# Optimization experiments

Hardware: AMD Instinct MI355X
Metric: run time of the kernel (lower is better)

Reference implementation:

```python
import jax, jax.numpy as jnp
import numpy as np
import math

EMBED_DIM = 1024
NUM_HEADS = 16
HEAD_DIM = EMBED_DIM // NUM_HEADS
BLOCK_SIZE = 64
NUM_RAND_BLOCKS = 3
B, L = 2, 2048


def _build_sparse_mask(seq_len, block_size, num_rand_blocks, seed=0):
    """BigBird block-sparse mask: global (first/last block) + window (prev/self/next) + random blocks."""
    nb = seq_len // block_size
    bm = np.zeros((nb, nb), dtype=bool)
    # global: first and last blocks attend to all / are attended by all
    bm[0, :] = True
    bm[:, 0] = True
    bm[-1, :] = True
    bm[:, -1] = True
    # sliding window for interior blocks
    for b in range(1, nb - 1):
        bm[b, max(b - 1, 0):b + 2] = True
    # random blocks for interior blocks (deterministic for reproducibility)
    rng = np.random.default_rng(seed)
    for b in range(1, nb - 1):
        avail = [x for x in range(nb) if x != b]
        picks = rng.permutation(len(avail))[:num_rand_blocks]
        for p in picks:
            bm[b, avail[p]] = True
    # expand block mask to token-level [L, L]
    return np.kron(bm, np.ones((block_size, block_size), dtype=bool))


def setup_inputs() -> dict:
    key = jax.random.key(0)
    k0, k1, k2, k3, k4 = jax.random.split(key, 5)
    hidden_states = jax.random.normal(k0, (B, L, EMBED_DIM), dtype=jnp.float32)
    s = 0.02
    # torch nn.Linear weights have shape [out_features, in_features]
    Wq = jax.random.normal(k1, (EMBED_DIM, EMBED_DIM), dtype=jnp.float32) * s
    Wk = jax.random.normal(k2, (EMBED_DIM, EMBED_DIM), dtype=jnp.float32) * s
    Wv = jax.random.normal(k3, (EMBED_DIM, EMBED_DIM), dtype=jnp.float32) * s
    Wo = jax.random.normal(k4, (EMBED_DIM, EMBED_DIM), dtype=jnp.float32) * s
    sparse_mask = jnp.asarray(_build_sparse_mask(L, BLOCK_SIZE, NUM_RAND_BLOCKS))
    return {"hidden_states": hidden_states, "Wq": Wq, "Wk": Wk, "Wv": Wv,
            "Wo": Wo, "sparse_mask": sparse_mask}


def reference(hidden_states, Wq, Wk, Wv, Wo, sparse_mask):
    Bsz, Lq, D = hidden_states.shape
    H, hd = NUM_HEADS, HEAD_DIM
    # projections (Linear no bias): x @ W.T
    q = (hidden_states @ Wq.T).reshape(Bsz, Lq, H, hd).transpose(0, 2, 1, 3)
    k = (hidden_states @ Wk.T).reshape(Bsz, Lq, H, hd).transpose(0, 2, 1, 3)
    v = (hidden_states @ Wv.T).reshape(Bsz, Lq, H, hd).transpose(0, 2, 1, 3)
    # dense scores with block-sparse mask (matches reference module's math)
    scores = jnp.einsum('bhqd,bhkd->bhqk', q, k) / math.sqrt(hd)  # [B,H,L,L]
    scores = jnp.where(sparse_mask[None, None, :, :], scores, -jnp.inf)
    attn = jax.nn.softmax(scores.astype(jnp.float32), axis=-1).astype(scores.dtype)
    out = jnp.einsum('bhqk,bhkd->bhqd', attn, v)
    out = out.transpose(0, 2, 1, 3).reshape(Bsz, Lq, D)
    out = out @ Wo.T
    return out
```

## Files before the change

kernel.cpp:

```cpp
#include <hip/hip_runtime.h>
#include <hip/hip_bf16.h>
#include <stdint.h>

#define LSEQ   2048
#define DMODEL 1024
#define NHEADS 16
#define HDIM   64
#define NB     32
#define BATCH  2
#define NGRP   38
#define NWG_ATTN (32 * NGRP)

typedef unsigned short u16;
typedef __attribute__((ext_vector_type(8))) __bf16 bf16x8;
typedef __attribute__((ext_vector_type(4))) float f32x4;
typedef __attribute__((ext_vector_type(4))) unsigned int u32x4;
typedef __attribute__((ext_vector_type(4))) u16 u16x4;


__device__ __forceinline__ u16 f2b(float f) {
  unsigned b = __float_as_uint(f);
  return (u16)((b + 0x7FFFu + ((b >> 16) & 1u)) >> 16);
}

__device__ __forceinline__ void lds_dma16(const u16* g, u16* l) {
  __builtin_amdgcn_global_load_lds(
      (__attribute__((address_space(1))) const void*)g,
      (__attribute__((address_space(3))) void*)l, 16, 0, 0);
}

__device__ __forceinline__ bool probe_is_bf16(const void* src) {
  const u16* p = (const u16*)src;
  int cnt = 0;
  #pragma unroll
  for (int i = 0; i < 64; ++i) {
    int e = (p[i] >> 7) & 0xFF;
    cnt += (e >= 100 && e <= 140) ? 1 : 0;
  }
  return cnt >= 48;
}

__device__ __forceinline__ bool mask_block(const void* m, int qb, int kb) {
  const unsigned char* p = (const unsigned char*)m;
  size_t e = (size_t)(qb * 64) * LSEQ + (size_t)kb * 64;
  unsigned char b0 = p[0], b1 = p[1], b2 = p[2];
  if (b0 == 1 && b1 == 1) return p[e] != 0;
  if (b0 == 1 && b1 == 0 && b2 == 1) return ((const u16*)m)[e] != 0;
  if (b0 == 1) return ((const unsigned int*)m)[e] != 0;
  if (b0 == 0x80 && b1 == 0x3f) return ((const u16*)m)[e] != 0;
  return ((const float*)m)[e] != 0.0f;
}

__global__ __launch_bounds__(256) void convert_kernel(
    const void* __restrict__ hs, const void* __restrict__ wq,
    const void* __restrict__ wk, const void* __restrict__ wv,
    const void* __restrict__ wo, u16* __restrict__ dst,
    const void* __restrict__ mask, int* __restrict__ skb,
    f32x4* __restrict__ zbuf, int zn4) {
  __shared__ int sflag;
  if (threadIdx.x == 0) sflag = probe_is_bf16(hs) ? 1 : 0;
  __syncthreads();
  bool isbf = sflag != 0;
  if (blockIdx.x == 0 && threadIdx.x < NB) {
    int qb = threadIdx.x;
    int base = (qb == 0) ? 0 : ((qb == 31) ? 32 : (64 + (qb - 1) * 8));
    int cap = (qb == 0 || qb == 31) ? 32 : 8;
    int c = 0;
    for (int kb = 0; kb < NB; ++kb)
      if (mask_block(mask, qb, kb)) skb[base + c++] = kb;
    for (; c < cap; ++c) skb[base + c] = -1;
  }
  const int HS4 = BATCH * LSEQ * DMODEL / 4;
  const int W4 = DMODEL * DMODEL / 4;
  int total4 = HS4 + 4 * W4;
  int stride = gridDim.x * blockDim.x;
  for (int i = blockIdx.x * blockDim.x + threadIdx.x; i < total4; i += stride) {
    const void* src;
    int off;
    if (i < HS4) { src = hs; off = i; }
    else {
      int j = i - HS4;
      int wsel = j >> 18;
      off = j & (W4 - 1);
      src = (wsel == 0) ? wq : (wsel == 1) ? wk : (wsel == 2) ? wv : wo;
    }
    u16x4 v;
    if (isbf) v = ((const u16x4*)src)[off];
    else {
      f32x4 f = ((const f32x4*)src)[off];
      v = (u16x4){f2b(f[0]), f2b(f[1]), f2b(f[2]), f2b(f[3])};
    }
    ((u16x4*)dst)[i] = v;
  }
  for (int i = blockIdx.x * blockDim.x + threadIdx.x; i < zn4; i += stride)
    zbuf[i] = (f32x4){0.f, 0.f, 0.f, 0.f};
}

#define QBM 256
#define QBN 256
#define QBK 64

#define BAR()  __builtin_amdgcn_s_barrier()
#define LGK0() asm volatile("s_waitcnt lgkmcnt(0)" ::: "memory")
#define VM4()  asm volatile("s_waitcnt vmcnt(4)" ::: "memory")
#define VM0()  asm volatile("s_waitcnt vmcnt(0)" ::: "memory")

#define STG_A(p, h, kt) do { \
    lds_dma16(Abase + ((h)*128 +  0)*1024 + (kt)*64, sA + (p)*16384 + (h)*8192 +        wb8); \
    lds_dma16(Abase + ((h)*128 + 64)*1024 + (kt)*64, sA + (p)*16384 + (h)*8192 + 4096 + wb8); \
  } while (0)
#define STG_B(p, h, kt) do { \
    lds_dma16(Bbase + ((h)*128 +  0)*1024 + (kt)*64, sB + (p)*16384 + (h)*8192 +        wb8); \
    lds_dma16(Bbase + ((h)*128 + 64)*1024 + (kt)*64, sB + (p)*16384 + (h)*8192 + 4096 + wb8); \
  } while (0)

#define LDA(p, mh) do { \
    const u16* _ba = sA + (p)*16384 + (wr*128 + (mh)*64 + lc)*64; \
    af[0][0] = *(const bf16x8*)(_ba +        x0); af[0][1] = *(const bf16x8*)(_ba +        x1); \
    af[1][0] = *(const bf16x8*)(_ba + 1024 + x0); af[1][1] = *(const bf16x8*)(_ba + 1024 + x1); \
    af[2][0] = *(const bf16x8*)(_ba + 2048 + x0); af[2][1] = *(const bf16x8*)(_ba + 2048 + x1); \
    af[3][0] = *(const bf16x8*)(_ba + 3072 + x0); af[3][1] = *(const bf16x8*)(_ba + 3072 + x1); \
  } while (0)
#define LDB(p, nh) do { \
    const u16* _bb = sB + (p)*16384 + (wc*64 + (nh)*32 + lc)*64; \
    bfr[nh][0][0] = *(const bf16x8*)(_bb +        x0); bfr[nh][0][1] = *(const bf16x8*)(_bb +        x1); \
    bfr[nh][1][0] = *(const bf16x8*)(_bb + 1024 + x0); bfr[nh][1][1] = *(const bf16x8*)(_bb + 1024 + x1); \
  } while (0)

#define MMQ(mh, nh) do { \
    __builtin_amdgcn_s_setprio(1); \
    _Pragma("unroll") \
    for (int _m = 0; _m < 4; ++_m) { \
      _Pragma("unroll") \
      for (int _n = 0; _n < 2; ++_n) { \
        f32x4 _c = acc[(mh)*4+_m][(nh)*2+_n]; \
        _c = __builtin_amdgcn_mfma_f32_16x16x32_bf16(af[_m][0], bfr[nh][_n][0], _c, 0, 0, 0); \
        _c = __builtin_amdgcn_mfma_f32_16x16x32_bf16(af[_m][1], bfr[nh][_n][1], _c, 0, 0, 0); \
        acc[(mh)*4+_m][(nh)*2+_n] = _c; \
      } \
    } \
    __builtin_amdgcn_s_setprio(0); \
  } while (0)

__global__ __launch_bounds__(512, 2) void gemm_qkv(
    const u16* __restrict__ A, const u16* __restrict__ Bw,
    u16* __restrict__ C, u16* __restrict__ C2) {
  extern __shared__ u16 smem[];
  u16* sA = smem;
  u16* sB = smem + 2 * 16384;

  const int t = threadIdx.x;
  const int l = t & 63;
  const int w = t >> 6;
  const int wr = w >> 2;
  const int wc = w & 3;
  const int q4 = l >> 4, lc = l & 15;
  const int tileM = blockIdx.x * QBM;
  const int tileN = blockIdx.y * QBN;
  const int sr = t >> 3;
  const int scs = (((t & 7) ^ ((t >> 3) & 7)) * 8);
  const int wb8 = w * 512;
  const int x0 = (q4 ^ (lc & 7)) * 8;
  const int x1 = x0 ^ 32;

  const u16* Abase = A + (size_t)(tileM + sr) * 1024 + scs;
  const u16* Bbase = Bw + (size_t)(tileN + sr) * 1024 + scs;

  f32x4 acc[8][4] = {};
  bf16x8 af[4][2];
  bf16x8 bfr[2][2][2];

  STG_B(0, 0, 0); STG_B(0, 1, 0);
  STG_A(0, 0, 0); STG_A(0, 1, 0);
  STG_B(1, 0, 1); STG_B(1, 1, 1);
  VM4(); BAR();

  #pragma unroll 1
  for (int j = 0; j < 7; ++j) {
    const int kt0 = 2 * j, kt1 = 2 * j + 1;
    LDA(0, 0); LDB(0, 0); STG_A(1, 0, kt1);
    BAR(); LGK0(); MMQ(0, 0); BAR();
    LDB(0, 1); STG_A(1, 1, kt1);
    BAR(); LGK0(); MMQ(0, 1); BAR();
    LDA(0, 1); STG_B(0, 0, kt0 + 2);
    BAR(); LGK0(); MMQ(1, 1); BAR();
    STG_B(0, 1, kt0 + 2);
    VM4(); BAR(); MMQ(1, 0); BAR();
    LDA(1, 0); LDB(1, 0); STG_A(0, 0, kt0 + 2);
    BAR(); LGK0(); MMQ(0, 0); BAR();
    LDB(1, 1); STG_A(0, 1, kt0 + 2);
    BAR(); LGK0(); MMQ(0, 1); BAR();
    LDA(1, 1); STG_B(1, 0, kt1 + 2);
    BAR(); LGK0(); MMQ(1, 1); BAR();
    STG_B(1, 1, kt1 + 2);
    VM4(); BAR(); MMQ(1, 0); BAR();
  }

  LDA(0, 0); LDB(0, 0); STG_A(1, 0, 15);
  BAR(); LGK0(); MMQ(0, 0); BAR();
  LDB(0, 1); STG_A(1, 1, 15);
  BAR(); LGK0(); MMQ(0, 1); BAR();
  LDA(0, 1);
  BAR(); LGK0(); MMQ(1, 1); BAR();
  VM0(); BAR(); MMQ(1, 0); BAR();
  LDA(1, 0); LDB(1, 0);
  BAR(); LGK0(); MMQ(0, 0); BAR();
  LDB(1, 1);
  BAR(); LGK0(); MMQ(0, 1); BAR();
  LDA(1, 1);
  LGK0(); MMQ(1, 1);
  MMQ(1, 0);

  #pragma unroll
  for (int im = 0; im < 8; ++im)
    #pragma unroll
    for (int jn = 0; jn < 4; ++jn) {
      int rowb = tileM + wr * 128 + im * 16 + q4 * 4;
      int col = tileN + wc * 64 + jn * 16 + lc;
      int sel = col >> 10;
      int o = col & 1023;
      int h = o >> 6, d = o & 63;
      int b = rowb >> 11, ll = rowb & 2047;
      if (sel == 2) {
        u16x4 pk = {f2b(acc[im][jn][0]), f2b(acc[im][jn][1]),
                    f2b(acc[im][jn][2]), f2b(acc[im][jn][3])};
        *(u16x4*)(C2 + ((size_t)((b * NHEADS + h) * HDIM + d)) * LSEQ + ll) = pk;
      } else {
        float scl = (sel == 0) ? 0.125f : 1.0f;
        #pragma unroll
        for (int r = 0; r < 4; ++r) {
          size_t idx = (size_t)sel * (size_t)(BATCH * NHEADS * LSEQ * HDIM) +
                       (((size_t)(b * NHEADS + h) * LSEQ) + ll + r) * HDIM + d;
          C[idx] = f2b(acc[im][jn][r] * scl);
        }
      }
    }
}

#define GTM 128
#define GTN 128
#define GBK 32
#define LDSW 32

__global__ __launch_bounds__(256) void gemm_bt(
    const u16* __restrict__ A, const u16* __restrict__ Bw,
    void* __restrict__ C, u16* __restrict__ C2, int M, int N, int K,
    int layout, int is_final, const void* __restrict__ probe_src) {
  __shared__ u16 lA[GTM * LDSW];
  __shared__ u16 lB[GTN * LDSW];
  __shared__ int sflag;
  int t = threadIdx.x;
  int w = t >> 6, l = t & 63, q4 = l >> 4, lc = l & 15;
  int lr = l >> 2, lcc = l & 3;
  int tileM = blockIdx.x * GTM, tileN = blockIdx.y * GTN;
  int wm = (w >> 1) * 64, wn = (w & 1) * 64;
  if (t == 0) sflag = (is_final && !probe_is_bf16(probe_src)) ? 0 : 1;

  f32x4 acc[4][4] = {};

  for (int kt = 0; kt < K; kt += GBK) {
    __syncthreads();
    #pragma unroll
    for (int it = 0; it < 2; ++it) {
      int m = w * 2 + it;
      int row = m * 16 + lr;
      lds_dma16(A + (size_t)(tileM + row) * K + kt + lcc * 8, lA + m * 512);
      lds_dma16(Bw + (size_t)(tileN + row) * K + kt + lcc * 8, lB + m * 512);
    }
    __syncthreads();
    bf16x8 af[4], bf[4];
    #pragma unroll
    for (int i = 0; i < 4; ++i)
      af[i] = *(const bf16x8*)(lA + (wm + i * 16 + lc) * LDSW + q4 * 8);
    #pragma unroll
    for (int j = 0; j < 4; ++j)
      bf[j] = *(const bf16x8*)(lB + (wn + j * 16 + lc) * LDSW + q4 * 8);
    #pragma unroll
    for (int i = 0; i < 4; ++i)
      #pragma unroll
      for (int j = 0; j < 4; ++j)
        acc[i][j] = __builtin_amdgcn_mfma_f32_16x16x32_bf16(af[i], bf[j], acc[i][j], 0, 0, 0);
  }

  bool out_bf = sflag != 0;
  #pragma unroll
  for (int i = 0; i < 4; ++i)
    #pragma unroll
    for (int j = 0; j < 4; ++j) {
      int rowb = tileM + wm + i * 16 + q4 * 4;
      int col = tileN + wn + j * 16 + lc;
      if (layout == 0) {
        #pragma unroll
        for (int r = 0; r < 4; ++r) {
          float v = acc[i][j][r];
          size_t idx = (size_t)(rowb + r) * N + col;
          if (out_bf) ((u16*)C)[idx] = f2b(v);
          else ((float*)C)[idx] = v;
        }
      } else {
        int sel = col >> 10;
        int o = col & 1023;
        int h = o >> 6, d = o & 63;
        int b = rowb >> 11, ll = rowb & 2047;
        if (sel == 2) {
          u16x4 pk = {f2b(acc[i][j][0]), f2b(acc[i][j][1]),
                      f2b(acc[i][j][2]), f2b(acc[i][j][3])};
          *(u16x4*)(C2 + ((size_t)((b * NHEADS + h) * HDIM + d)) * LSEQ + ll) = pk;
        } else {
          float sc = (sel == 0) ? 0.125f : 1.0f;
          #pragma unroll
          for (int r = 0; r < 4; ++r) {
            size_t idx = (size_t)sel * (size_t)(BATCH * NHEADS * LSEQ * HDIM) +
                         (((size_t)(b * NHEADS + h) * LSEQ) + ll + r) * HDIM + d;
            ((u16*)C)[idx] = f2b(acc[i][j][r] * sc);
          }
        }
      }
    }
}

#define LDP 72

__global__ __launch_bounds__(256) void attn_kernel(
    const u16* __restrict__ qb_, const u16* __restrict__ kb_,
    const u16* __restrict__ vt_, const int* __restrict__ skb,
    float* __restrict__ obuf2, float* __restrict__ lbuf2,
    u16* __restrict__ ctx) {
  __shared__ u16 lK[2][64 * 64];
  __shared__ u16 lV[2][64 * 64];
  __shared__ u16 lP[4][16 * LDP];
  int i = blockIdx.x;
  int bh = (i & 7) + ((i >> 3) & 3) * 8;
  int g = i >> 5;
  int qb = (g < 4) ? 0 : ((g < 8) ? 31 : (g - 7));
  int t = threadIdx.x, w = t >> 6, l = t & 63, q4 = l >> 4, lc = l & 15;
  int r0 = t >> 3, r1 = 32 + (t >> 3);
  int scc = ((t & 7) ^ ((t >> 3) & 7)) * 8;
  const int x0 = (q4 ^ (lc & 7)) * 8;
  const int x1 = x0 ^ 32;

  const u16* qp = qb_ + ((size_t)bh * LSEQ + qb * 64 + w * 16 + lc) * HDIM;
  bf16x8 bq0 = *(const bf16x8*)(qp + q4 * 8);
  bf16x8 bq1 = *(const bf16x8*)(qp + 32 + q4 * 8);

  const u16* kp = kb_ + (size_t)bh * LSEQ * HDIM;
  const u16* vp = vt_ + (size_t)bh * HDIM * LSEQ;
  u16* myP = &lP[w][0];

  f32x4 oacc[4];
  #pragma unroll
  for (int d = 0; d < 4; ++d) oacc[d] = (f32x4){0.f, 0.f, 0.f, 0.f};
  float lp = 0.0f;

  int nkb = 0;
  #pragma unroll
  for (int j = 0; j < 8; ++j) nkb += (skb[g * 8 + j] >= 0) ? 1 : 0;

  auto STAGE = [&](int it, int buf) {
    int kb = skb[g * 8 + it];
    const u16* kblk = kp + (size_t)kb * 64 * HDIM;
    const u16* vblk = vp + kb * 64;
    u16* dK = &lK[buf][0];
    u16* dV = &lV[buf][0];
    lds_dma16(kblk + r0 * HDIM + scc, dK + w * 512);
    lds_dma16(kblk + r1 * HDIM + scc, dK + 2048 + w * 512);
    lds_dma16(vblk + (size_t)r0 * LSEQ + scc, dV + w * 512);
    lds_dma16(vblk + (size_t)r1 * LSEQ + scc, dV + 2048 + w * 512);
  };

  STAGE(0, 0);
  __syncthreads();

  for (int it = 0; it < nkb; ++it) {
    int buf = it & 1;
    if (it + 1 < nkb) STAGE(it + 1, buf ^ 1);
    const u16* bK = &lK[buf][0];
    const u16* bV = &lV[buf][0];

    f32x4 st[4];
    #pragma unroll
    for (int mt = 0; mt < 4; ++mt) {
      const u16* kr = bK + (mt * 16 + lc) * 64;
      bf16x8 k0 = *(const bf16x8*)(kr + x0);
      bf16x8 k1 = *(const bf16x8*)(kr + x1);
      f32x4 z = (f32x4){0.f, 0.f, 0.f, 0.f};
      z = __builtin_amdgcn_mfma_f32_16x16x32_bf16(k0, bq0, z, 0, 0, 0);
      z = __builtin_amdgcn_mfma_f32_16x16x32_bf16(k1, bq1, z, 0, 0, 0);
      st[mt] = z;
    }

    #pragma unroll
    for (int mt = 0; mt < 4; ++mt) {
      float p0 = __expf(st[mt][0]), p1 = __expf(st[mt][1]);
      float p2 = __expf(st[mt][2]), p3 = __expf(st[mt][3]);
      lp += (p0 + p1) + (p2 + p3);
      u16x4 pk = {f2b(p0), f2b(p1), f2b(p2), f2b(p3)};
      *(u16x4*)(myP + lc * LDP + mt * 16 + q4 * 4) = pk;
    }

    bf16x8 ap0 = *(const bf16x8*)(myP + lc * LDP + q4 * 8);
    bf16x8 ap1 = *(const bf16x8*)(myP + lc * LDP + 32 + q4 * 8);
    #pragma unroll
    for (int dt = 0; dt < 4; ++dt) {
      const u16* vr = bV + (dt * 16 + lc) * 64;
      bf16x8 v0 = *(const bf16x8*)(vr + x0);
      bf16x8 v1 = *(const bf16x8*)(vr + x1);
      oacc[dt] = __builtin_amdgcn_mfma_f32_16x16x32_bf16(ap0, v0, oacc[dt], 0, 0, 0);
      oacc[dt] = __builtin_amdgcn_mfma_f32_16x16x32_bf16(ap1, v1, oacc[dt], 0, 0, 0);
    }

    __syncthreads();
  }

  float ltot = lp;
  ltot += __shfl_xor(ltot, 16);
  ltot += __shfl_xor(ltot, 32);

  if (g >= 8) {
    float inv[4];
    #pragma unroll
    for (int r = 0; r < 4; ++r)
      inv[r] = 1.0f / __shfl(ltot, q4 * 4 + r);
    int b = bh >> 4, h = bh & 15;
    #pragma unroll
    for (int dt = 0; dt < 4; ++dt)
      #pragma unroll
      for (int r = 0; r < 4; ++r) {
        float v = oacc[dt][r] * inv[r];
        int grow = qb * 64 + w * 16 + q4 * 4 + r;
        size_t odx = ((size_t)b * LSEQ + grow) * DMODEL + h * HDIM + dt * 16 + lc;
        ctx[odx] = f2b(v);
      }
  } else {
    int s = (qb == 31) ? 1 : 0;
    if (q4 == 0)
      unsafeAtomicAdd(lbuf2 + ((size_t)bh * 2 + s) * 64 + w * 16 + lc, ltot);
    #pragma unroll
    for (int dt = 0; dt < 4; ++dt)
      #pragma unroll
      for (int r = 0; r < 4; ++r)
        unsafeAtomicAdd(obuf2 + (((size_t)bh * 2 + s) * 64 + w * 16 + q4 * 4 + r) * 64 +
                            dt * 16 + lc, oacc[dt][r]);
  }
}

__global__ __launch_bounds__(256) void normalize2_kernel(
    const float* __restrict__ obuf2, const float* __restrict__ lbuf2,
    u16* __restrict__ ctx) {
  int e4 = blockIdx.x * 256 + threadIdx.x;
  int e = e4 * 4;
  int bh = e >> 13;
  int rem = e & 8191;
  int s = rem >> 12, row = (rem >> 6) & 63, d = rem & 63;
  f32x4 o = *(const f32x4*)(obuf2 + e);
  float linv = 1.0f / lbuf2[(bh * 2 + s) * 64 + row];
  int qb = s ? 31 : 0;
  int b = bh >> 4, h = bh & 15;
  int grow = qb * 64 + row;
  u16x4 pk = {f2b(o[0] * linv), f2b(o[1] * linv), f2b(o[2] * linv), f2b(o[3] * linv)};
  *(u16x4*)(ctx + ((size_t)b * LSEQ + grow) * DMODEL + h * HDIM + d) = pk;
}

extern "C" void kernel_launch(void* const* d_in, const int* in_sizes, int n_in,
                              void* d_out, int out_size, void* d_ws, size_t ws_size,
                              hipStream_t stream) {
  const void* hs = d_in[0];
  const void* wq = d_in[1];
  const void* wk = d_in[2];
  const void* wv = d_in[3];
  const void* wo = d_in[4];
  const void* mask = d_in[5];

  u16* hsb = (u16*)d_ws;
  u16* wqb = hsb + 4 * 1024 * 1024;
  u16* wob = wqb + 3 * 1024 * 1024;
  u16* qbuf = wob + 1024 * 1024;
  u16* kbuf = qbuf + 4 * 1024 * 1024;
  u16* vtb  = kbuf + 4 * 1024 * 1024;
  u16* ctx  = vtb + 4 * 1024 * 1024;
  int* skb  = (int*)(ctx + 4 * 1024 * 1024);
  float* obuf2 = (float*)(skb + 512);
  float* lbuf2 = obuf2 + 32 * 2 * 64 * 64;
  const int ZN4 = (32 * 2 * 64 * 64 + 4096) / 4;

  static bool attr_done = false;
  if (!attr_done) {
    hipFuncSetAttribute((const void*)gemm_qkv,
                        hipFuncAttributeMaxDynamicSharedMemorySize, 131072);
    attr_done = true;
  }

  convert_kernel<<<4096, 256, 0, stream>>>(hs, wq, wk, wv, wo, hsb, mask, skb,
                                           (f32x4*)obuf2, ZN4);

  dim3 gqkv(16, 12);
  gemm_qkv<<<gqkv, 512, 131072, stream>>>(hsb, wqb, qbuf, vtb);

  attn_kernel<<<NWG_ATTN, 256, 0, stream>>>(qbuf, kbuf, vtb, skb, obuf2, lbuf2, ctx);

  normalize2_kernel<<<256, 256, 0, stream>>>(obuf2, lbuf2, ctx);

  dim3 gout(32, 8);
  gemm_bt<<<gout, 256, 0, stream>>>(ctx, wob, d_out, nullptr, 4096, 1024, 1024, 0, 1, hs);
}
```

Measured before the change: 199.3 us.

## Skip bf16 conversion copies by reading raw inputs directly; retile output GEMM

The conversion kernel now probes hidden states and weights separately and skips copying any input that is already bf16. The QKV and output GEMMs read those raw buffers directly when they are bf16. The output projection moves from 128x128 to 128x64 tiles, doubling the workgroup count to improve occupancy on the 1024-wide output. If the test inputs are fp32, only the tile change matters and every GEMM workgroup pays extra probe overhead.

```diff
diff --git a/kernel.cpp b/kernel.cpp
--- a/kernel.cpp
+++ b/kernel.cpp
@@ -57,10 +57,11 @@
     const void* __restrict__ wo, u16* __restrict__ dst,
     const void* __restrict__ mask, int* __restrict__ skb,
     f32x4* __restrict__ zbuf, int zn4) {
-  __shared__ int sflag;
-  if (threadIdx.x == 0) sflag = probe_is_bf16(hs) ? 1 : 0;
+  __shared__ int sflags;
+  if (threadIdx.x == 0)
+    sflags = (probe_is_bf16(hs) ? 1 : 0) | (probe_is_bf16(wq) ? 2 : 0);
   __syncthreads();
-  bool isbf = sflag != 0;
+  bool bf_hs = (sflags & 1) != 0, bf_w = (sflags & 2) != 0;
   if (blockIdx.x == 0 && threadIdx.x < NB) {
     int qb = threadIdx.x;
     int base = (qb == 0) ? 0 : ((qb == 31) ? 32 : (64 + (qb - 1) * 8));
@@ -74,23 +75,23 @@
   const int W4 = DMODEL * DMODEL / 4;
   int total4 = HS4 + 4 * W4;
   int stride = gridDim.x * blockDim.x;
-  for (int i = blockIdx.x * blockDim.x + threadIdx.x; i < total4; i += stride) {
-    const void* src;
-    int off;
-    if (i < HS4) { src = hs; off = i; }
-    else {
-      int j = i - HS4;
-      int wsel = j >> 18;
-      off = j & (W4 - 1);
-      src = (wsel == 0) ? wq : (wsel == 1) ? wk : (wsel == 2) ? wv : wo;
-    }
-    u16x4 v;
-    if (isbf) v = ((const u16x4*)src)[off];
-    else {
+  if (!(bf_hs && bf_w)) {
+    for (int i = blockIdx.x * blockDim.x + threadIdx.x; i < total4; i += stride) {
+      const void* src;
+      int off;
+      bool isbf;
+      if (i < HS4) { src = hs; off = i; isbf = bf_hs; }
+      else {
+        int j = i - HS4;
+        int wsel = j >> 18;
+        off = j & (W4 - 1);
+        src = (wsel == 0) ? wq : (wsel == 1) ? wk : (wsel == 2) ? wv : wo;
+        isbf = bf_w;
+      }
+      if (isbf) continue;
       f32x4 f = ((const f32x4*)src)[off];
-      v = (u16x4){f2b(f[0]), f2b(f[1]), f2b(f[2]), f2b(f[3])};
-    }
-    ((u16x4*)dst)[i] = v;
+      ((u16x4*)dst)[i] = (u16x4){f2b(f[0]), f2b(f[1]), f2b(f[2]), f2b(f[3])};
+    }
   }
   for (int i = blockIdx.x * blockDim.x + threadIdx.x; i < zn4; i += stride)
     zbuf[i] = (f32x4){0.f, 0.f, 0.f, 0.f};
@@ -143,7 +144,9 @@
   } while (0)
 
 __global__ __launch_bounds__(512, 2) void gemm_qkv(
-    const u16* __restrict__ A, const u16* __restrict__ Bw,
+    const void* __restrict__ hs_raw, const u16* __restrict__ hs_cv,
+    const void* __restrict__ wq_r, const void* __restrict__ wk_r,
+    const void* __restrict__ wv_r, const u16* __restrict__ wqb_cv,
     u16* __restrict__ C, u16* __restrict__ C2) {
   extern __shared__ u16 smem[];
   u16* sA = smem;
@@ -163,8 +166,16 @@
   const int x0 = (q4 ^ (lc & 7)) * 8;
   const int x1 = x0 ^ 32;
 
-  const u16* Abase = A + (size_t)(tileM + sr) * 1024 + scs;
-  const u16* Bbase = Bw + (size_t)(tileN + sr) * 1024 + scs;
+  const bool a_bf = probe_is_bf16(hs_raw);
+  const bool b_bf = probe_is_bf16(wq_r);
+  const u16* Asrc = a_bf ? (const u16*)hs_raw : hs_cv;
+  const int wsel = tileN >> 10;
+  const void* wraw = (wsel == 0) ? wq_r : (wsel == 1) ? wk_r : wv_r;
+  const u16* Bsrc = b_bf ? (const u16*)wraw + (size_t)(tileN & 1023) * 1024
+                         : wqb_cv + (size_t)tileN * 1024;
+
+  const u16* Abase = Asrc + (size_t)(tileM + sr) * 1024 + scs;
+  const u16* Bbase = Bsrc + (size_t)sr * 1024 + scs;
 
   f32x4 acc[8][4] = {};
   bf16x8 af[4][2];
@@ -237,84 +248,63 @@
     }
 }
 
-#define GTM 128
-#define GTN 128
-#define GBK 32
-#define LDSW 32
-
-__global__ __launch_bounds__(256) void gemm_bt(
-    const u16* __restrict__ A, const u16* __restrict__ Bw,
-    void* __restrict__ C, u16* __restrict__ C2, int M, int N, int K,
-    int layout, int is_final, const void* __restrict__ probe_src) {
-  __shared__ u16 lA[GTM * LDSW];
-  __shared__ u16 lB[GTN * LDSW];
-  __shared__ int sflag;
+#define OTK 32
+
+__global__ __launch_bounds__(256) void gemm_out(
+    const u16* __restrict__ A, const void* __restrict__ wo_raw,
+    const u16* __restrict__ wo_cv, void* __restrict__ C,
+    const void* __restrict__ probe_src) {
+  __shared__ u16 lA[128 * OTK];
+  __shared__ u16 lB[64 * OTK];
   int t = threadIdx.x;
   int w = t >> 6, l = t & 63, q4 = l >> 4, lc = l & 15;
   int lr = l >> 2, lcc = l & 3;
-  int tileM = blockIdx.x * GTM, tileN = blockIdx.y * GTN;
-  int wm = (w >> 1) * 64, wn = (w & 1) * 64;
-  if (t == 0) sflag = (is_final && !probe_is_bf16(probe_src)) ? 0 : 1;
-
-  f32x4 acc[4][4] = {};
-
-  for (int kt = 0; kt < K; kt += GBK) {
+  int tileM = blockIdx.x * 128, tileN = blockIdx.y * 64;
+  int wm = (w >> 1) * 64, wn = (w & 1) * 32;
+  bool out_bf = probe_is_bf16(probe_src);
+  const u16* Bsrc = probe_is_bf16(wo_raw) ? (const u16*)wo_raw : wo_cv;
+
+  f32x4 acc[4][2] = {};
+
+  for (int kt = 0; kt < 1024; kt += OTK) {
     __syncthreads();
     #pragma unroll
     for (int it = 0; it < 2; ++it) {
       int m = w * 2 + it;
       int row = m * 16 + lr;
-      lds_dma16(A + (size_t)(tileM + row) * K + kt + lcc * 8, lA + m * 512);
-      lds_dma16(Bw + (size_t)(tileN + row) * K + kt + lcc * 8, lB + m * 512);
+      lds_dma16(A + (size_t)(tileM + row) * 1024 + kt + lcc * 8, lA + m * 512);
+    }
+    {
+      int row = w * 16 + lr;
+      lds_dma16(Bsrc + (size_t)(tileN + row) * 1024 + kt + lcc * 8, lB + w * 512);
     }
     __syncthreads();
-    bf16x8 af[4], bf[4];
+    bf16x8 af[4], bf[2];
     #pragma unroll
     for (int i = 0; i < 4; ++i)
-      af[i] = *(const bf16x8*)(lA + (wm + i * 16 + lc) * LDSW + q4 * 8);
-    #pragma unroll
-    for (int j = 0; j < 4; ++j)
-      bf[j] = *(const bf16x8*)(lB + (wn + j * 16 + lc) * LDSW + q4 * 8);
+      af[i] = *(const bf16x8*)(lA + (wm + i * 16 + lc) * OTK + q4 * 8);
+    #pragma unroll
+    for (int j = 0; j < 2; ++j)
+      bf[j] = *(const bf16x8*)(lB + (wn + j * 16 + lc) * OTK + q4 * 8);
     #pragma unroll
     for (int i = 0; i < 4; ++i)
       #pragma unroll
-      for (int j = 0; j < 4; ++j)
+      for (int j = 0; j < 2; ++j)
         acc[i][j] = __builtin_amdgcn_mfma_f32_16x16x32_bf16(af[i], bf[j], acc[i][j], 0, 0, 0);
   }
 
-  bool out_bf = sflag != 0;
   #pragma unroll
   for (int i = 0; i < 4; ++i)
     #pragma unroll
-    for (int j = 0; j < 4; ++j) {
+    for (int j = 0; j < 2; ++j) {
       int rowb = tileM + wm + i * 16 + q4 * 4;
       int col = tileN + wn + j * 16 + lc;
-      if (layout == 0) {
-        #pragma unroll
-        for (int r = 0; r < 4; ++r) {
-          float v = acc[i][j][r];
-          size_t idx = (size_t)(rowb + r) * N + col;
-          if (out_bf) ((u16*)C)[idx] = f2b(v);
-          else ((float*)C)[idx] = v;
-        }
-      } else {
-        int sel = col >> 10;
-        int o = col & 1023;
-        int h = o >> 6, d = o & 63;
-        int b = rowb >> 11, ll = rowb & 2047;
-        if (sel == 2) {
-          u16x4 pk = {f2b(acc[i][j][0]), f2b(acc[i][j][1]),
-                      f2b(acc[i][j][2]), f2b(acc[i][j][3])};
-          *(u16x4*)(C2 + ((size_t)((b * NHEADS + h) * HDIM + d)) * LSEQ + ll) = pk;
-        } else {
-          float sc = (sel == 0) ? 0.125f : 1.0f;
-          #pragma unroll
-          for (int r = 0; r < 4; ++r) {
-            size_t idx = (size_t)sel * (size_t)(BATCH * NHEADS * LSEQ * HDIM) +
-                         (((size_t)(b * NHEADS + h) * LSEQ) + ll + r) * HDIM + d;
-            ((u16*)C)[idx] = f2b(acc[i][j][r] * sc);
-          }
-        }
+      #pragma unroll
+      for (int r = 0; r < 4; ++r) {
+        float v = acc[i][j][r];
+        size_t idx = (size_t)(rowb + r) * 1024 + col;
+        if (out_bf) ((u16*)C)[idx] = f2b(v);
+        else ((float*)C)[idx] = v;
       }
     }
 }
@@ -494,12 +484,12 @@
                                            (f32x4*)obuf2, ZN4);
 
   dim3 gqkv(16, 12);
-  gemm_qkv<<<gqkv, 512, 131072, stream>>>(hsb, wqb, qbuf, vtb);
+  gemm_qkv<<<gqkv, 512, 131072, stream>>>(hs, hsb, wq, wk, wv, wqb, qbuf, vtb);
 
   attn_kernel<<<NWG_ATTN, 256, 0, stream>>>(qbuf, kbuf, vtb, skb, obuf2, lbuf2, ctx);
 
   normalize2_kernel<<<256, 256, 0, stream>>>(obuf2, lbuf2, ctx);
 
-  dim3 gout(32, 8);
-  gemm_bt<<<gout, 256, 0, stream>>>(ctx, wob, d_out, nullptr, 4096, 1024, 1024, 0, 1, hs);
-}
+  dim3 gout(32, 16);
+  gemm_out<<<gout, 256, 0, stream>>>(ctx, wo, wob, d_out, hs);
+}
```

Result: no change. 199.5 us (+0.1%).
